# Kernel optimization log

Hardware: AMD Instinct MI355X
Metric: run time of the kernel (lower is better)

## Reference

```python
import jax, jax.numpy as jnp
import numpy as np
import math

NUM_LEVELS = 12
FEAT = 2
LOG2_HASH = 17
HASH_SIZE = 2 ** LOG2_HASH
BASE_RES = 16
FINEST_RES = 256
N_POINTS = 1_000_000

_b = math.exp((math.log(FINEST_RES) - math.log(BASE_RES)) / (NUM_LEVELS - 1))
# static per-level grid resolutions, matching max(1, int(round(base * b**lvl)))
RESOLUTIONS = np.array([max(1, int(round(BASE_RES * _b ** l))) for l in range(NUM_LEVELS)], dtype=np.float32)
PRIMES = np.array([73856093, 19349663, 83492791], dtype=np.int32)
# the 8 trilinear corner offsets, ordered (ix, iy, iz) as in the torch loops
OFFSETS = np.array([[ix, iy, iz] for ix in (0, 1) for iy in (0, 1) for iz in (0, 1)], dtype=np.int32)


def setup_inputs() -> dict:
    key = jax.random.key(0)
    k1, k2 = jax.random.split(key)
    x = jax.random.uniform(k1, (N_POINTS, 3), dtype=jnp.float32)  # canonical coords in [0,1)
    # stacked embedding tables, init uniform(-1e-4, 1e-4) per reset_parameters
    tables = jax.random.uniform(k2, (NUM_LEVELS, HASH_SIZE, FEAT), dtype=jnp.float32,
                                minval=-1e-4, maxval=1e-4)
    return {"x": x, "tables": tables}


def reference(x, tables):
    # x: [N, 3], tables: [L, H, F] -> out: [N, L, F]
    res = jnp.asarray(RESOLUTIONS)                       # [L]
    xs = x[:, None, :] * res[None, :, None]              # [N, L, 3]
    x0f = jnp.floor(xs)
    w = xs - x0f                                         # [N, L, 3]
    x0 = x0f.astype(jnp.int32)

    offs = jnp.asarray(OFFSETS)                          # [8, 3]
    corners = x0[:, :, None, :] + offs[None, None, :, :] # [N, L, 8, 3]
    primes = jnp.asarray(PRIMES)
    # spatial hash; int32 wraparound is harmless since HASH_SIZE is a power of 2
    # dividing 2^32, so h & (HASH_SIZE-1) == torch.remainder(int64 hash, HASH_SIZE)
    h = (corners[..., 0] * primes[0]) ^ (corners[..., 1] * primes[1]) ^ (corners[..., 2] * primes[2])
    idx = h & (HASH_SIZE - 1)                            # [N, L, 8]

    lvl = jnp.arange(NUM_LEVELS)[None, :, None]          # broadcast level index
    feats = tables[lvl, idx]                             # [N, L, 8, F]

    offs_f = offs.astype(jnp.float32)                    # [8, 3]
    # trilinear weight per corner: prod over axes of (w if offset==1 else 1-w)
    wts = jnp.prod(jnp.where(offs_f[None, None, :, :] > 0,
                             w[:, :, None, :], 1.0 - w[:, :, None, :]), axis=-1)  # [N, L, 8]

    return jnp.einsum('nlc,nlcf->nlf', wts, feats)       # [N, L, F]
```

## Files before the change

### kernel.cpp

```cpp
#include <hip/hip_runtime.h>
#include <cstdint>

constexpr int kHashSize = 1 << 17;
constexpr uint32_t kHashMask = (uint32_t)kHashSize - 1u;
constexpr int kBuckets = 32 * 32 * 32;

typedef float f2 __attribute__((ext_vector_type(2)));
typedef float f4 __attribute__((ext_vector_type(4)));

__global__ __launch_bounds__(256) void k_zero(uint32_t* hist) {
  int i = blockIdx.x * 256 + threadIdx.x;
  if (i < kBuckets) hist[i] = 0u;
}

__global__ __launch_bounds__(256) void k_hist(const float* __restrict__ x,
                                              uint32_t* __restrict__ hist,
                                              uint32_t* __restrict__ cellbuf,
                                              uint32_t* __restrict__ rankbuf,
                                              int npts) {
  int n = blockIdx.x * 256 + threadIdx.x;
  if (n >= npts) return;
  float px = x[3 * n + 0], py = x[3 * n + 1], pz = x[3 * n + 2];
  uint32_t ix = (uint32_t)min(31, (int)(px * 32.f));
  uint32_t iy = (uint32_t)min(31, (int)(py * 32.f));
  uint32_t iz = (uint32_t)min(31, (int)(pz * 32.f));
  uint32_t cell = (ix << 10) | (iy << 5) | iz;
  uint32_t r = atomicAdd(&hist[cell], 1u);
  cellbuf[n] = cell;
  rankbuf[n] = r;
}

__global__ __launch_bounds__(1024) void k_scan(uint32_t* __restrict__ hist) {
  __shared__ uint32_t lds[1024];
  const int t = threadIdx.x;
  uint32_t v[32];
  uint32_t s = 0;
#pragma unroll
  for (int i = 0; i < 32; ++i) {
    v[i] = hist[t * 32 + i];
    s += v[i];
  }
  lds[t] = s;
  __syncthreads();
  for (int off = 1; off < 1024; off <<= 1) {
    uint32_t add = (t >= off) ? lds[t - off] : 0u;
    __syncthreads();
    lds[t] += add;
    __syncthreads();
  }
  uint32_t run = lds[t] - s;
#pragma unroll
  for (int i = 0; i < 32; ++i) {
    uint32_t c = v[i];
    hist[t * 32 + i] = run;
    run += c;
  }
}

__global__ __launch_bounds__(256) void k_scatter(const float* __restrict__ x,
                                                 const uint32_t* __restrict__ offs,
                                                 const uint32_t* __restrict__ cellbuf,
                                                 const uint32_t* __restrict__ rankbuf,
                                                 f4* __restrict__ pts, int npts) {
  int n = blockIdx.x * 256 + threadIdx.x;
  if (n >= npts) return;
  uint32_t pos = offs[cellbuf[n]] + rankbuf[n];
  f4 p;
  p.x = x[3 * n + 0];
  p.y = x[3 * n + 1];
  p.z = x[3 * n + 2];
  p.w = __uint_as_float((uint32_t)n);
  pts[pos] = p;
}

__global__ __launch_bounds__(256) void hashenc_main(
    const f4* __restrict__ pts,
    const float* __restrict__ tables,
    float* __restrict__ out,
    int npts) {
  const float kRes[12] = {16.f,  21.f,  26.f,  34.f,  44.f,  56.f,
                          73.f,  93.f,  120.f, 155.f, 199.f, 256.f};
  int n = blockIdx.x * 256 + threadIdx.x;
  if (n >= npts) return;

  const f4 p = pts[n];
  const float px = p.x, py = p.y, pz = p.z;
  const uint32_t orig = __float_as_uint(p.w);

  const f2* __restrict__ tbl2 = reinterpret_cast<const f2*>(tables);

  float acc[12][2];

#pragma unroll
  for (int l = 0; l < 12; ++l) {
    const float r = kRes[l];
    const float xs = px * r, ys = py * r, zs = pz * r;
    const float fx = floorf(xs), fy = floorf(ys), fz = floorf(zs);
    const float wx = xs - fx, wy = ys - fy, wz = zs - fz;
    const uint32_t ix = (uint32_t)(int32_t)fx;
    const uint32_t iy = (uint32_t)(int32_t)fy;
    const uint32_t iz = (uint32_t)(int32_t)fz;

    const uint32_t hx0 = ix * 73856093u, hx1 = hx0 + 73856093u;
    const uint32_t hy0 = iy * 19349663u, hy1 = hy0 + 19349663u;
    const uint32_t hz0 = iz * 83492791u, hz1 = hz0 + 83492791u;

    const f2* __restrict__ t = tbl2 + (size_t)l * kHashSize;

    const f2 f000 = t[(hx0 ^ hy0 ^ hz0) & kHashMask];
    const f2 f001 = t[(hx0 ^ hy0 ^ hz1) & kHashMask];
    const f2 f010 = t[(hx0 ^ hy1 ^ hz0) & kHashMask];
    const f2 f011 = t[(hx0 ^ hy1 ^ hz1) & kHashMask];
    const f2 f100 = t[(hx1 ^ hy0 ^ hz0) & kHashMask];
    const f2 f101 = t[(hx1 ^ hy0 ^ hz1) & kHashMask];
    const f2 f110 = t[(hx1 ^ hy1 ^ hz0) & kHashMask];
    const f2 f111 = t[(hx1 ^ hy1 ^ hz1) & kHashMask];

    const float ax0 = 1.f - wx, ax1 = wx;
    const float by0 = 1.f - wy, by1 = wy;
    const float cz0 = 1.f - wz, cz1 = wz;
    const float ab00 = ax0 * by0, ab01 = ax0 * by1;
    const float ab10 = ax1 * by0, ab11 = ax1 * by1;
    const float w000 = ab00 * cz0, w001 = ab00 * cz1;
    const float w010 = ab01 * cz0, w011 = ab01 * cz1;
    const float w100 = ab10 * cz0, w101 = ab10 * cz1;
    const float w110 = ab11 * cz0, w111 = ab11 * cz1;

    acc[l][0] = w000 * f000.x + w001 * f001.x + w010 * f010.x + w011 * f011.x +
                w100 * f100.x + w101 * f101.x + w110 * f110.x + w111 * f111.x;
    acc[l][1] = w000 * f000.y + w001 * f001.y + w010 * f010.y + w011 * f011.y +
                w100 * f100.y + w101 * f101.y + w110 * f110.y + w111 * f111.y;
  }

  f4* o = reinterpret_cast<f4*>(out + (size_t)orig * 24);
#pragma unroll
  for (int k = 0; k < 6; ++k) {
    f4 v;
    v.x = acc[2 * k + 0][0];
    v.y = acc[2 * k + 0][1];
    v.z = acc[2 * k + 1][0];
    v.w = acc[2 * k + 1][1];
    __builtin_nontemporal_store(v, o + k);
  }
}

__global__ __launch_bounds__(256) void hashenc_grouped(
    const float* __restrict__ x, const float* __restrict__ tables,
    float* __restrict__ out, int npts, int bpg) {
  const float kRes[12] = {16.f,  21.f,  26.f,  34.f,  44.f,  56.f,
                          73.f,  93.f,  120.f, 155.f, 199.f, 256.f};
  const int b = blockIdx.x;
  const int c = b & 7;
  const int g = c >> 1;
  const int sub = ((b >> 3) << 1) | (c & 1);
  if (sub >= bpg) return;
  const int n = sub * 256 + (int)threadIdx.x;
  if (n >= npts) return;
  const float px = x[3 * n + 0], py = x[3 * n + 1], pz = x[3 * n + 2];
  const f2* __restrict__ tbl2 = reinterpret_cast<const f2*>(tables);
  f2 accv[3];
#pragma unroll
  for (int k = 0; k < 3; ++k) {
    const int l = 3 * g + k;
    const float r = kRes[l];
    const float xs = px * r, ys = py * r, zs = pz * r;
    const float fx = floorf(xs), fy = floorf(ys), fz = floorf(zs);
    const float wx = xs - fx, wy = ys - fy, wz = zs - fz;
    const uint32_t ix = (uint32_t)(int32_t)fx;
    const uint32_t iy = (uint32_t)(int32_t)fy;
    const uint32_t iz = (uint32_t)(int32_t)fz;
    const uint32_t hx0 = ix * 73856093u, hx1 = hx0 + 73856093u;
    const uint32_t hy0 = iy * 19349663u, hy1 = hy0 + 19349663u;
    const uint32_t hz0 = iz * 83492791u, hz1 = hz0 + 83492791u;
    const f2* __restrict__ t = tbl2 + (size_t)l * kHashSize;
    const f2 f000 = t[(hx0 ^ hy0 ^ hz0) & kHashMask];
    const f2 f001 = t[(hx0 ^ hy0 ^ hz1) & kHashMask];
    const f2 f010 = t[(hx0 ^ hy1 ^ hz0) & kHashMask];
    const f2 f011 = t[(hx0 ^ hy1 ^ hz1) & kHashMask];
    const f2 f100 = t[(hx1 ^ hy0 ^ hz0) & kHashMask];
    const f2 f101 = t[(hx1 ^ hy0 ^ hz1) & kHashMask];
    const f2 f110 = t[(hx1 ^ hy1 ^ hz0) & kHashMask];
    const f2 f111 = t[(hx1 ^ hy1 ^ hz1) & kHashMask];
    const float ax0 = 1.f - wx, ax1 = wx;
    const float by0 = 1.f - wy, by1 = wy;
    const float cz0 = 1.f - wz, cz1 = wz;
    const float ab00 = ax0 * by0, ab01 = ax0 * by1;
    const float ab10 = ax1 * by0, ab11 = ax1 * by1;
    const float w000 = ab00 * cz0, w001 = ab00 * cz1;
    const float w010 = ab01 * cz0, w011 = ab01 * cz1;
    const float w100 = ab10 * cz0, w101 = ab10 * cz1;
    const float w110 = ab11 * cz0, w111 = ab11 * cz1;
    f2 a;
    a.x = w000 * f000.x + w001 * f001.x + w010 * f010.x + w011 * f011.x +
          w100 * f100.x + w101 * f101.x + w110 * f110.x + w111 * f111.x;
    a.y = w000 * f000.y + w001 * f001.y + w010 * f010.y + w011 * f011.y +
          w100 * f100.y + w101 * f101.y + w110 * f110.y + w111 * f111.y;
    accv[k] = a;
  }
  f2* o = reinterpret_cast<f2*>(out + (size_t)n * 24 + g * 6);
  __builtin_nontemporal_store(accv[0], o + 0);
  __builtin_nontemporal_store(accv[1], o + 1);
  __builtin_nontemporal_store(accv[2], o + 2);
}

extern "C" void kernel_launch(void* const* d_in, const int* in_sizes, int n_in,
                              void* d_out, int out_size, void* d_ws, size_t ws_size,
                              hipStream_t stream) {
  const float* x = (const float*)d_in[0];
  const float* tables = (const float*)d_in[1];
  float* out = (float*)d_out;
  const int npts = in_sizes[0] / 3;
  const int nb = (npts + 255) / 256;

  const size_t npad = (size_t)nb * 256;
  const size_t off_cell = 1u << 20;
  const size_t off_rank = off_cell + 4 * npad;
  const size_t off_pts = off_cell + 8 * npad;
  const size_t need = off_cell + 24 * npad;

  if (ws_size >= need) {
    uint8_t* ws = (uint8_t*)d_ws;
    uint32_t* hist = (uint32_t*)ws;
    uint32_t* cellbuf = (uint32_t*)(ws + off_cell);
    uint32_t* rankbuf = (uint32_t*)(ws + off_rank);
    f4* pts = (f4*)(ws + off_pts);

    hipLaunchKernelGGL(k_zero, dim3((kBuckets + 255) / 256), dim3(256), 0,
                       stream, hist);
    hipLaunchKernelGGL(k_hist, dim3(nb), dim3(256), 0, stream, x, hist, cellbuf,
                       rankbuf, npts);
    hipLaunchKernelGGL(k_scan, dim3(1), dim3(1024), 0, stream, hist);
    hipLaunchKernelGGL(k_scatter, dim3(nb), dim3(256), 0, stream, x, hist,
                       cellbuf, rankbuf, pts, npts);
    hipLaunchKernelGGL(hashenc_main, dim3(nb), dim3(256), 0, stream, pts,
                       tables, out, npts);
  } else {
    const int bpg = nb;
    const int nblocks = 8 * ((bpg + 1) / 2);
    hipLaunchKernelGGL(hashenc_grouped, dim3(nblocks), dim3(256), 0, stream, x,
                       tables, out, npts, bpg);
  }
}
```

Before: 516.4 us.

## Drop cell/rank buffers, scatter via atomic offsets, remap blocks across XCDs

The histogram pass no longer stores per-point cell and rank arrays. The scatter pass recomputes each cell and takes its slot with an atomicAdd on the prefix-summed offsets, which removes 8 bytes per point of workspace writes and reads. The change also vectorizes the x loads to four points per thread, replaces the zero kernel with a memset, moves the resolutions into constant memory, and remaps hashenc_main block indices so each XCD (selected by blockIdx mod 8) works on a contiguous run of sorted blocks for better L2 locality. Within a cell, point order now follows atomic arrival order rather than the histogram rank, which does not affect correctness.

```diff
diff --git a/kernel.cpp b/kernel.cpp
--- a/kernel.cpp
+++ b/kernel.cpp
@@ -8,37 +8,44 @@
 typedef float f2 __attribute__((ext_vector_type(2)));
 typedef float f4 __attribute__((ext_vector_type(4)));
 
-__global__ __launch_bounds__(256) void k_zero(uint32_t* hist) {
-  int i = blockIdx.x * 256 + threadIdx.x;
-  if (i < kBuckets) hist[i] = 0u;
-}
-
-__global__ __launch_bounds__(256) void k_hist(const float* __restrict__ x,
-                                              uint32_t* __restrict__ hist,
-                                              uint32_t* __restrict__ cellbuf,
-                                              uint32_t* __restrict__ rankbuf,
-                                              int npts) {
-  int n = blockIdx.x * 256 + threadIdx.x;
-  if (n >= npts) return;
-  float px = x[3 * n + 0], py = x[3 * n + 1], pz = x[3 * n + 2];
+__constant__ float kRes[12] = {16.f,  21.f,  26.f,  34.f,  44.f,  56.f,
+                               73.f,  93.f,  120.f, 155.f, 199.f, 256.f};
+
+__device__ __forceinline__ uint32_t cell_of(float px, float py, float pz) {
   uint32_t ix = (uint32_t)min(31, (int)(px * 32.f));
   uint32_t iy = (uint32_t)min(31, (int)(py * 32.f));
   uint32_t iz = (uint32_t)min(31, (int)(pz * 32.f));
-  uint32_t cell = (ix << 10) | (iy << 5) | iz;
-  uint32_t r = atomicAdd(&hist[cell], 1u);
-  cellbuf[n] = cell;
-  rankbuf[n] = r;
+  return (ix << 10) | (iy << 5) | iz;
+}
+
+__global__ __launch_bounds__(256) void k_hist(const float* __restrict__ x,
+                                              uint32_t* __restrict__ hist,
+                                              int npts) {
+  int i = blockIdx.x * 256 + threadIdx.x;
+  int n0 = i * 4;
+  if (n0 + 3 < npts) {
+    const f4* xv = reinterpret_cast<const f4*>(x + 3 * n0);
+    f4 a = xv[0], b = xv[1], c = xv[2];
+    atomicAdd(&hist[cell_of(a.x, a.y, a.z)], 1u);
+    atomicAdd(&hist[cell_of(a.w, b.x, b.y)], 1u);
+    atomicAdd(&hist[cell_of(b.z, b.w, c.x)], 1u);
+    atomicAdd(&hist[cell_of(c.y, c.z, c.w)], 1u);
+  } else {
+    for (int n = n0; n < npts; ++n)
+      atomicAdd(&hist[cell_of(x[3 * n], x[3 * n + 1], x[3 * n + 2])], 1u);
+  }
 }
 
 __global__ __launch_bounds__(1024) void k_scan(uint32_t* __restrict__ hist) {
   __shared__ uint32_t lds[1024];
   const int t = threadIdx.x;
-  uint32_t v[32];
+  uint4 v[8];
   uint32_t s = 0;
-#pragma unroll
-  for (int i = 0; i < 32; ++i) {
-    v[i] = hist[t * 32 + i];
-    s += v[i];
+  const uint4* h4 = reinterpret_cast<const uint4*>(hist) + t * 8;
+#pragma unroll
+  for (int i = 0; i < 8; ++i) {
+    v[i] = h4[i];
+    s += v[i].x + v[i].y + v[i].z + v[i].w;
   }
   lds[t] = s;
   __syncthreads();
@@ -49,38 +56,59 @@
     __syncthreads();
   }
   uint32_t run = lds[t] - s;
-#pragma unroll
-  for (int i = 0; i < 32; ++i) {
-    uint32_t c = v[i];
-    hist[t * 32 + i] = run;
-    run += c;
+  uint4* o4 = reinterpret_cast<uint4*>(hist) + t * 8;
+#pragma unroll
+  for (int i = 0; i < 8; ++i) {
+    uint4 w;
+    w.x = run; run += v[i].x;
+    w.y = run; run += v[i].y;
+    w.z = run; run += v[i].z;
+    w.w = run; run += v[i].w;
+    o4[i] = w;
   }
 }
 
 __global__ __launch_bounds__(256) void k_scatter(const float* __restrict__ x,
-                                                 const uint32_t* __restrict__ offs,
-                                                 const uint32_t* __restrict__ cellbuf,
-                                                 const uint32_t* __restrict__ rankbuf,
+                                                 uint32_t* __restrict__ hist,
                                                  f4* __restrict__ pts, int npts) {
-  int n = blockIdx.x * 256 + threadIdx.x;
-  if (n >= npts) return;
-  uint32_t pos = offs[cellbuf[n]] + rankbuf[n];
-  f4 p;
-  p.x = x[3 * n + 0];
-  p.y = x[3 * n + 1];
-  p.z = x[3 * n + 2];
-  p.w = __uint_as_float((uint32_t)n);
-  pts[pos] = p;
+  int i = blockIdx.x * 256 + threadIdx.x;
+  int n0 = i * 4;
+  if (n0 + 3 < npts) {
+    const f4* xv = reinterpret_cast<const f4*>(x + 3 * n0);
+    f4 a = xv[0], b = xv[1], c = xv[2];
+    float px[4] = {a.x, a.w, b.z, c.y};
+    float py[4] = {a.y, b.x, b.w, c.z};
+    float pz[4] = {a.z, b.y, c.x, c.w};
+#pragma unroll
+    for (int k = 0; k < 4; ++k) {
+      uint32_t pos = atomicAdd(&hist[cell_of(px[k], py[k], pz[k])], 1u);
+      f4 p;
+      p.x = px[k]; p.y = py[k]; p.z = pz[k];
+      p.w = __uint_as_float((uint32_t)(n0 + k));
+      pts[pos] = p;
+    }
+  } else {
+    for (int n = n0; n < npts; ++n) {
+      f4 p;
+      p.x = x[3 * n + 0]; p.y = x[3 * n + 1]; p.z = x[3 * n + 2];
+      p.w = __uint_as_float((uint32_t)n);
+      uint32_t pos = atomicAdd(&hist[cell_of(p.x, p.y, p.z)], 1u);
+      pts[pos] = p;
+    }
+  }
 }
 
 __global__ __launch_bounds__(256) void hashenc_main(
     const f4* __restrict__ pts,
     const float* __restrict__ tables,
     float* __restrict__ out,
-    int npts) {
-  const float kRes[12] = {16.f,  21.f,  26.f,  34.f,  44.f,  56.f,
-                          73.f,  93.f,  120.f, 155.f, 199.f, 256.f};
-  int n = blockIdx.x * 256 + threadIdx.x;
+    int npts, int nb8, int nb) {
+  const int b = blockIdx.x;
+  const int c = b & 7;
+  const int r = b >> 3;
+  const int pblk = c * nb8 + r;
+  if (pblk >= nb) return;
+  const int n = pblk * 256 + (int)threadIdx.x;
   if (n >= npts) return;
 
   const f4 p = pts[n];
@@ -93,8 +121,8 @@
 
 #pragma unroll
   for (int l = 0; l < 12; ++l) {
-    const float r = kRes[l];
-    const float xs = px * r, ys = py * r, zs = pz * r;
+    const float rr = kRes[l];
+    const float xs = px * rr, ys = py * rr, zs = pz * rr;
     const float fx = floorf(xs), fy = floorf(ys), fz = floorf(zs);
     const float wx = xs - fx, wy = ys - fy, wz = zs - fz;
     const uint32_t ix = (uint32_t)(int32_t)fx;
@@ -147,8 +175,6 @@
 __global__ __launch_bounds__(256) void hashenc_grouped(
     const float* __restrict__ x, const float* __restrict__ tables,
     float* __restrict__ out, int npts, int bpg) {
-  const float kRes[12] = {16.f,  21.f,  26.f,  34.f,  44.f,  56.f,
-                          73.f,  93.f,  120.f, 155.f, 199.f, 256.f};
   const int b = blockIdx.x;
   const int c = b & 7;
   const int g = c >> 1;
@@ -162,8 +188,8 @@
 #pragma unroll
   for (int k = 0; k < 3; ++k) {
     const int l = 3 * g + k;
-    const float r = kRes[l];
-    const float xs = px * r, ys = py * r, zs = pz * r;
+    const float rr = kRes[l];
+    const float xs = px * rr, ys = py * rr, zs = pz * rr;
     const float fx = floorf(xs), fy = floorf(ys), fz = floorf(zs);
     const float wx = xs - fx, wy = ys - fy, wz = zs - fz;
     const uint32_t ix = (uint32_t)(int32_t)fx;
@@ -211,29 +237,25 @@
   float* out = (float*)d_out;
   const int npts = in_sizes[0] / 3;
   const int nb = (npts + 255) / 256;
+  const int nb8 = (nb + 7) / 8;
 
   const size_t npad = (size_t)nb * 256;
-  const size_t off_cell = 1u << 20;
-  const size_t off_rank = off_cell + 4 * npad;
-  const size_t off_pts = off_cell + 8 * npad;
-  const size_t need = off_cell + 24 * npad;
+  const size_t off_pts = 1u << 20;
+  const size_t need = off_pts + 16 * npad;
 
   if (ws_size >= need) {
     uint8_t* ws = (uint8_t*)d_ws;
     uint32_t* hist = (uint32_t*)ws;
-    uint32_t* cellbuf = (uint32_t*)(ws + off_cell);
-    uint32_t* rankbuf = (uint32_t*)(ws + off_rank);
     f4* pts = (f4*)(ws + off_pts);
 
-    hipLaunchKernelGGL(k_zero, dim3((kBuckets + 255) / 256), dim3(256), 0,
-                       stream, hist);
-    hipLaunchKernelGGL(k_hist, dim3(nb), dim3(256), 0, stream, x, hist, cellbuf,
-                       rankbuf, npts);
+    hipMemsetAsync(hist, 0, kBuckets * sizeof(uint32_t), stream);
+    const int nq = ((npts + 3) / 4 + 255) / 256;
+    hipLaunchKernelGGL(k_hist, dim3(nq), dim3(256), 0, stream, x, hist, npts);
     hipLaunchKernelGGL(k_scan, dim3(1), dim3(1024), 0, stream, hist);
-    hipLaunchKernelGGL(k_scatter, dim3(nb), dim3(256), 0, stream, x, hist,
-                       cellbuf, rankbuf, pts, npts);
-    hipLaunchKernelGGL(hashenc_main, dim3(nb), dim3(256), 0, stream, pts,
-                       tables, out, npts);
+    hipLaunchKernelGGL(k_scatter, dim3(nq), dim3(256), 0, stream, x, hist, pts,
+                       npts);
+    hipLaunchKernelGGL(hashenc_main, dim3(8 * nb8), dim3(256), 0, stream, pts,
+                       tables, out, npts, nb8, nb);
   } else {
     const int bpg = nb;
     const int nblocks = 8 * ((bpg + 1) / 2);
```

After: 569.2 us. +10.2%, slower.
